# Kernel optimization log

Hardware: AMD Instinct MI355X
Metric: run time of the kernel (lower is better)

Reference implementation:

```python
import jax, jax.numpy as jnp
import numpy as np

N_NODES = 10000
N_EDGES = 640000
NODE_DIM = 128
EDGE_DIM = 32
OUT_DIM = 128


def setup_inputs() -> dict:
    key = jax.random.key(0)
    k_h, k_e, k_ef, k_w1, k_w2 = jax.random.split(key, 5)
    h = jax.random.normal(k_h, (N_NODES, NODE_DIM), dtype=jnp.float32)
    edge_index = jax.random.randint(k_e, (2, N_EDGES), 0, N_NODES, dtype=jnp.int64)
    edge_features = jax.random.normal(k_ef, (N_EDGES, EDGE_DIM), dtype=jnp.float32)
    in_dim = 2 * NODE_DIM + EDGE_DIM
    # Kaiming-ish init scale for realism
    W1 = jax.random.normal(k_w1, (in_dim, OUT_DIM), dtype=jnp.float32) / np.sqrt(in_dim)
    b1 = jnp.zeros((OUT_DIM,), dtype=jnp.float32)
    W2 = jax.random.normal(k_w2, (OUT_DIM, OUT_DIM), dtype=jnp.float32) / np.sqrt(OUT_DIM)
    b2 = jnp.zeros((OUT_DIM,), dtype=jnp.float32)
    return {"h": h, "edge_index": edge_index, "edge_features": edge_features,
            "n": N_NODES, "W1": W1, "b1": b1, "W2": W2, "b2": b2}


def reference(h, edge_index, edge_features, n, W1, b1, W2, b2):
    rows, cols = edge_index[0], edge_index[1]
    # gather source/target node features + edge features -> [E, 2*node_dim+edge_dim]
    msg_input = jnp.concatenate([h[rows], h[cols], edge_features], axis=-1)
    hidden = jax.nn.relu(msg_input @ W1 + b1)   # [E, out_dim]
    messages = hidden @ W2 + b2                 # [E, out_dim]
    # scatter-add messages onto destination rows -> [n, out_dim]
    out = jax.ops.segment_sum(messages, rows, num_segments=n)
    return out
```

## Files before the change

### kernel.cpp

```cpp
#include <hip/hip_runtime.h>
#include <hip/hip_bf16.h>


typedef __attribute__((ext_vector_type(8))) short bf16x8;
typedef __attribute__((ext_vector_type(4))) float f32x4;

#define ND 128
#define ED 32
#define CH 64

__device__ __forceinline__ short f2bf(float x) {
  unsigned int u = __float_as_uint(x);
  unsigned int r = (u + 0x7FFFu + ((u >> 16) & 1u)) >> 16;
  return (short)r;
}

__device__ __forceinline__ float bf2f(short s) {
  return __uint_as_float(((unsigned int)(unsigned short)s) << 16);
}

__device__ __forceinline__ f32x4 bf8lo(bf16x8 v) {
  f32x4 r;
  #pragma unroll
  for (int j = 0; j < 4; ++j) r[j] = bf2f(v[j]);
  return r;
}
__device__ __forceinline__ f32x4 bf8hi(bf16x8 v) {
  f32x4 r;
  #pragma unroll
  for (int j = 0; j < 4; ++j) r[j] = bf2f(v[4 + j]);
  return r;
}

__device__ __forceinline__ int load_idx(const void* ei, long long i, int is64) {
  return is64 ? (int)((const long long*)ei)[i] : ((const int*)ei)[i];
}

__device__ __forceinline__ int swz(int c) {
  int ct = c >> 4, cc = c & 15;
  return (ct >> 2) * 64 + (cc >> 2) * 16 + (ct & 3) * 4 + (cc & 3);
}

__global__ __launch_bounds__(256) void prep_kernel(
    const float* __restrict__ W1, const float* __restrict__ W2,
    const unsigned int* __restrict__ ei, short* __restrict__ w12t,
    short* __restrict__ w1eA, short* __restrict__ w2t, int* __restrict__ flag,
    int* __restrict__ counts, int N) {
  if (blockIdx.x == 0 && threadIdx.x == 0) {
    int is64 = 1;
    for (int i = 0; i < 16; ++i)
      if (ei[2 * i + 1] != 0u) is64 = 0;
    flag[0] = is64;
  }
  int t = blockIdx.x * blockDim.x + threadIdx.x;
  for (int i = t; i < N; i += 32768) counts[i] = 0;
  if (t < 256 * 128) {
    int np = t >> 7, k = t & 127;
    float v = (np < 128) ? W1[k * 128 + np] : W1[(128 + k) * 128 + (np - 128)];
    w12t[t] = f2bf(v);
  }
  if (t < 128 * 128) {
    int n = t >> 7, k = t & 127;
    w2t[t] = f2bf(W2[k * 128 + n]);
  }
  if (t < 8 * 64 * 8) {
    int ct = t >> 9, lane = (t >> 3) & 63, j = t & 7;
    int li = lane & 15, lg = lane >> 4;
    w1eA[t] = f2bf(W1[(256 + lg * 8 + j) * 128 + ct * 16 + li]);
  }
}

__global__ void hist_kernel(const void* __restrict__ ei, const int* __restrict__ flag,
                            int* __restrict__ counts, int* __restrict__ rank,
                            unsigned int* __restrict__ rc, int E) {
  int e = blockIdx.x * blockDim.x + threadIdx.x;
  if (e >= E) return;
  int f = flag[0];
  int r = load_idx(ei, e, f);
  int c = load_idx(ei, (long long)E + e, f);
  rank[e] = atomicAdd(&counts[r], 1);
  rc[e] = ((unsigned int)r << 16) | (unsigned int)c;
}

__global__ __launch_bounds__(1024) void scan_kernel(const int* __restrict__ counts,
                                                    int* __restrict__ row_ptr, int n) {
  __shared__ int wtot[16];
  int tid = threadIdx.x;
  int lane = tid & 63, w = tid >> 6;
  int base_i = tid * 16;
  int c[16];
  int tot = 0;
  #pragma unroll
  for (int j = 0; j < 16; ++j) {
    int i = base_i + j;
    c[j] = (i < n) ? counts[i] : 0;
    tot += c[j];
  }
  int x = tot;
  #pragma unroll
  for (int d = 1; d < 64; d <<= 1) {
    int t = __shfl_up(x, d);
    if (lane >= d) x += t;
  }
  if (lane == 63) wtot[w] = x;
  __syncthreads();
  if (w == 0) {
    int y = (lane < 16) ? wtot[lane] : 0;
    #pragma unroll
    for (int d = 1; d < 16; d <<= 1) {
      int t = __shfl_up(y, d);
      if (lane >= d) y += t;
    }
    if (lane < 16) wtot[lane] = y;
  }
  __syncthreads();
  int waveoff = (w == 0) ? 0 : wtot[w - 1];
  int run = waveoff + x - tot;
  if (tid == 0) row_ptr[0] = 0;
  #pragma unroll
  for (int j = 0; j < 16; ++j) {
    int i = base_i + j;
    if (i < n) {
      run += c[j];
      row_ptr[i + 1] = run;
    }
  }
}

__global__ __launch_bounds__(256, 4) void scatter_sg_kernel(
    const float* __restrict__ ef, const int* __restrict__ row_ptr,
    const int* __restrict__ rank, const unsigned int* __restrict__ rc,
    const float* __restrict__ h, const short* __restrict__ w12t,
    const float* __restrict__ b1, short* __restrict__ efb,
    unsigned short* __restrict__ ccol, int2* __restrict__ cb,
    float* __restrict__ s2, short* __restrict__ g2, int N, int E, int nchunks) {
  int b = blockIdx.x;
  int SGB = (N + 63) >> 6;
  int SCB = (4 * E + 255) >> 8;
  if (b < SGB) {
    int lane = threadIdx.x & 63, w = threadIdx.x >> 6;
    int li = lane & 15, lg = lane >> 4;
    int base = b * 64 + w * 16;
    int rowm = base + li;
    if (rowm >= N) rowm = N - 1;
    float breg[8];
    #pragma unroll
    for (int nt = 0; nt < 8; ++nt) breg[nt] = b1[nt * 16 + li];
    f32x4 acc[16];
    #pragma unroll
    for (int nt = 0; nt < 16; ++nt) acc[nt] = (f32x4){0.f, 0.f, 0.f, 0.f};
    #pragma unroll
    for (int kc = 0; kc < 4; ++kc) {
      f32x4 f0 = *(const f32x4*)(h + (size_t)rowm * ND + kc * 32 + lg * 8);
      f32x4 f1 = *(const f32x4*)(h + (size_t)rowm * ND + kc * 32 + lg * 8 + 4);
      bf16x8 a;
      #pragma unroll
      for (int j = 0; j < 4; ++j) { a[j] = f2bf(f0[j]); a[4 + j] = f2bf(f1[j]); }
      #pragma unroll
      for (int nt = 0; nt < 16; ++nt) {
        bf16x8 bb = *(const bf16x8*)(w12t + (nt * 16 + li) * 128 + kc * 32 + lg * 8);
        acc[nt] = __builtin_amdgcn_mfma_f32_16x16x32_bf16(a, bb, acc[nt], 0, 0, 0);
      }
    }
    #pragma unroll
    for (int nt = 0; nt < 16; ++nt)
      #pragma unroll
      for (int r = 0; r < 4; ++r) {
        int row = base + lg * 4 + r;
        if (row < N) {
          if (nt < 8) {
            s2[(size_t)row * 128 + swz(nt * 16 + li)] = acc[nt][r] + breg[nt];
          } else {
            g2[(size_t)row * 128 + swz((nt - 8) * 16 + li)] = f2bf(acc[nt][r]);
          }
        }
      }
  } else if (b < SGB + SCB) {
    int gt = (b - SGB) * 256 + threadIdx.x;
    int e = gt >> 2, part = gt & 3;
    if (e < E) {
      unsigned int p = rc[e];
      int r = (int)(p >> 16), c = (int)(p & 0xffffu);
      int pos = row_ptr[r] + rank[e];
      f32x4 a0 = *(const f32x4*)(ef + (size_t)e * ED + part * 8);
      f32x4 a1 = *(const f32x4*)(ef + (size_t)e * ED + part * 8 + 4);
      bf16x8 ob;
      #pragma unroll
      for (int j = 0; j < 4; ++j) { ob[j] = f2bf(a0[j]); ob[4 + j] = f2bf(a1[j]); }
      *(bf16x8*)(efb + (size_t)pos * ED + part * 8) = ob;
      if (part == 0) ccol[pos] = (unsigned short)c;
    }
  } else {
    int k = (b - SGB - SCB) * 256 + threadIdx.x;
    if (k < nchunks) {
      int t0 = k * CH, t1 = t0 + CH;
      int lo = 0, hi = N;
      while (lo < hi) { int mid = (lo + hi) >> 1; if (row_ptr[mid] < t0) lo = mid + 1; else hi = mid; }
      int na = lo;
      hi = N;
      while (lo < hi) { int mid = (lo + hi) >> 1; if (row_ptr[mid] < t1) lo = mid + 1; else hi = mid; }
      cb[k] = make_int2(na, lo);
    }
  }
}

__global__ __launch_bounds__(128, 4) void layer1_kernel(
    const float* __restrict__ s2, const short* __restrict__ g2,
    const short* __restrict__ efb, const unsigned short* __restrict__ ccol,
    const short* __restrict__ w1eA, const int* __restrict__ row_ptr,
    const int2* __restrict__ cb, float* __restrict__ hsum) {
  int2 bounds = cb[blockIdx.x];
  int na = bounds.x, nb = bounds.y;
  if (na >= nb) return;
  int lane = threadIdx.x & 63;
  int w = threadIdx.x >> 6;
  int li = lane & 15, lg = lane >> 4;

  bf16x8 wa[4];
  #pragma unroll
  for (int nt = 0; nt < 4; ++nt)
    wa[nt] = *(const bf16x8*)(w1eA + ((w * 4 + nt) * 64 + lane) * 8);

  for (int n = na; n < nb; ++n) {
    int rp = row_ptr[n], rpe = row_ptr[n + 1];
    int deg = rpe - rp;
    f32x4 sreg[4];
    #pragma unroll
    for (int nt = 0; nt < 4; ++nt)
      sreg[nt] = *(const f32x4*)(s2 + (size_t)n * 128 + w * 64 + lg * 16 + nt * 4);
    f32x4 psum[4];
    #pragma unroll
    for (int nt = 0; nt < 4; ++nt) psum[nt] = (f32x4){0.f, 0.f, 0.f, 0.f};

    int ntiles = (deg + 15) >> 4;
    int last = rpe - 1;
    auto ldpos = [&](int t) {
      int p = rp + t * 16 + li;
      return p > last ? last : p;
    };

    int pA = ldpos(0), pB = ldpos(1);
    int cA = ccol[pA], cB = ccol[pB];
    bf16x8 eA = *(const bf16x8*)(efb + (size_t)pA * ED + lg * 8);
    bf16x8 eB = *(const bf16x8*)(efb + (size_t)pB * ED + lg * 8);
    const short* gpA = g2 + (size_t)cA * 128 + w * 64 + lg * 16;
    bf16x8 gA0 = *(const bf16x8*)gpA;
    bf16x8 gA1 = *(const bf16x8*)(gpA + 8);

    for (int t = 0; t < ntiles; ++t) {
      const short* gpB = g2 + (size_t)cB * 128 + w * 64 + lg * 16;
      bf16x8 gB0 = *(const bf16x8*)gpB;
      bf16x8 gB1 = *(const bf16x8*)(gpB + 8);
      int pC = ldpos(t + 2);
      int cC = ccol[pC];
      bf16x8 eC = *(const bf16x8*)(efb + (size_t)pC * ED + lg * 8);
      f32x4 a0 = __builtin_amdgcn_mfma_f32_16x16x32_bf16(wa[0], eA, (f32x4){0.f,0.f,0.f,0.f}, 0, 0, 0);
      f32x4 a1 = __builtin_amdgcn_mfma_f32_16x16x32_bf16(wa[1], eA, (f32x4){0.f,0.f,0.f,0.f}, 0, 0, 0);
      f32x4 a2 = __builtin_amdgcn_mfma_f32_16x16x32_bf16(wa[2], eA, (f32x4){0.f,0.f,0.f,0.f}, 0, 0, 0);
      f32x4 a3 = __builtin_amdgcn_mfma_f32_16x16x32_bf16(wa[3], eA, (f32x4){0.f,0.f,0.f,0.f}, 0, 0, 0);
      if ((t * 16 + li) < deg) {
        f32x4 v0 = a0 + sreg[0] + bf8lo(gA0);
        f32x4 v1 = a1 + sreg[1] + bf8hi(gA0);
        f32x4 v2 = a2 + sreg[2] + bf8lo(gA1);
        f32x4 v3 = a3 + sreg[3] + bf8hi(gA1);
        #pragma unroll
        for (int r = 0; r < 4; ++r) {
          psum[0][r] += (v0[r] > 0.f ? v0[r] : 0.f);
          psum[1][r] += (v1[r] > 0.f ? v1[r] : 0.f);
          psum[2][r] += (v2[r] > 0.f ? v2[r] : 0.f);
          psum[3][r] += (v3[r] > 0.f ? v3[r] : 0.f);
        }
      }
      cB = cC; eA = eB; eB = eC;
      gA0 = gB0; gA1 = gB1;
    }

    #pragma unroll
    for (int nt = 0; nt < 4; ++nt)
      #pragma unroll
      for (int r = 0; r < 4; ++r) {
        float v = psum[nt][r];
        v += __shfl_xor(v, 1);
        v += __shfl_xor(v, 2);
        v += __shfl_xor(v, 4);
        v += __shfl_xor(v, 8);
        psum[nt][r] = v;
      }
    if (li == 0) {
      #pragma unroll
      for (int nt = 0; nt < 4; ++nt)
        *(f32x4*)(hsum + (size_t)n * 128 + w * 64 + nt * 16 + lg * 4) = psum[nt];
    }
  }
}

__global__ __launch_bounds__(256) void out_kernel(const float* __restrict__ hsum,
                                                  const short* __restrict__ w2t,
                                                  const float* __restrict__ b2,
                                                  const int* __restrict__ row_ptr,
                                                  float* __restrict__ out, int N) {
  int lane = threadIdx.x & 63, w = threadIdx.x >> 6;
  int li = lane & 15, lg = lane >> 4;
  int base = blockIdx.x * 64 + w * 16;
  int rowm = base + li;
  if (rowm >= N) rowm = N - 1;
  float breg[8];
  #pragma unroll
  for (int nt = 0; nt < 8; ++nt) breg[nt] = b2[nt * 16 + li];
  f32x4 acc[8];
  #pragma unroll
  for (int nt = 0; nt < 8; ++nt) acc[nt] = (f32x4){0.f, 0.f, 0.f, 0.f};
  #pragma unroll
  for (int kc = 0; kc < 4; ++kc) {
    f32x4 f0 = *(const f32x4*)(hsum + (size_t)rowm * 128 + kc * 32 + lg * 8);
    f32x4 f1 = *(const f32x4*)(hsum + (size_t)rowm * 128 + kc * 32 + lg * 8 + 4);
    bf16x8 a;
    #pragma unroll
    for (int j = 0; j < 4; ++j) { a[j] = f2bf(f0[j]); a[4 + j] = f2bf(f1[j]); }
    #pragma unroll
    for (int nt = 0; nt < 8; ++nt) {
      bf16x8 bb = *(const bf16x8*)(w2t + (nt * 16 + li) * 128 + kc * 32 + lg * 8);
      acc[nt] = __builtin_amdgcn_mfma_f32_16x16x32_bf16(a, bb, acc[nt], 0, 0, 0);
    }
  }
  #pragma unroll
  for (int r = 0; r < 4; ++r) {
    int row = base + lg * 4 + r;
    if (row < N) {
      float dg = (float)(row_ptr[row + 1] - row_ptr[row]);
      #pragma unroll
      for (int nt = 0; nt < 8; ++nt)
        out[(size_t)row * 128 + nt * 16 + li] = acc[nt][r] + dg * breg[nt];
    }
  }
}

extern "C" void kernel_launch(void* const* d_in, const int* in_sizes, int n_in,
                              void* d_out, int out_size, void* d_ws, size_t ws_size,
                              hipStream_t stream) {
  const float* h  = (const float*)d_in[0];
  const void*  ei = d_in[1];
  const float* ef = (const float*)d_in[2];
  const float* W1 = (const float*)d_in[4];
  const float* b1 = (const float*)d_in[5];
  const float* W2 = (const float*)d_in[6];
  const float* b2 = (const float*)d_in[7];
  float* out = (float*)d_out;
  int N = in_sizes[0] / ND;
  int E = in_sizes[2] / ED;
  int nchunks = (E + CH - 1) / CH;

  char* ws = (char*)d_ws;
  size_t off = 0;
  auto alloc = [&](size_t bytes) {
    size_t o = off;
    off = (off + bytes + 255) & ~(size_t)255;
    return o;
  };
  int*            flag    = (int*)(ws + alloc(4));
  int*            counts  = (int*)(ws + alloc((size_t)N * 4));
  int*            row_ptr = (int*)(ws + alloc((size_t)(N + 1) * 4));
  int*            rank    = (int*)(ws + alloc((size_t)E * 4));
  unsigned int*   rc      = (unsigned int*)(ws + alloc((size_t)E * 4));
  short*          w12t    = (short*)(ws + alloc(256 * 128 * 2));
  short*          w1eA    = (short*)(ws + alloc(8 * 64 * 8 * 2));
  short*          w2t     = (short*)(ws + alloc(128 * 128 * 2));
  float*          s2      = (float*)(ws + alloc((size_t)N * 128 * 4));
  short*          g2      = (short*)(ws + alloc((size_t)N * 128 * 2));
  float*          hsumb   = (float*)(ws + alloc((size_t)N * 128 * 4));
  short*          efb     = (short*)(ws + alloc((size_t)E * ED * 2));
  unsigned short* ccol    = (unsigned short*)(ws + alloc((size_t)E * 2));
  int2*           cbb     = (int2*)(ws + alloc((size_t)nchunks * 8));

  int SGB = (N + 63) >> 6;
  int SCB = (4 * E + 255) >> 8;
  int CBB = (nchunks + 255) >> 8;

  prep_kernel<<<128, 256, 0, stream>>>(W1, W2, (const unsigned int*)ei, w12t, w1eA, w2t,
                                       flag, counts, N);
  hist_kernel<<<(E + 255) / 256, 256, 0, stream>>>(ei, flag, counts, rank, rc, E);
  scan_kernel<<<1, 1024, 0, stream>>>(counts, row_ptr, N);
  scatter_sg_kernel<<<SGB + SCB + CBB, 256, 0, stream>>>(
      ef, row_ptr, rank, rc, h, w12t, b1, efb, ccol, cbb, s2, g2, N, E, nchunks);
  layer1_kernel<<<nchunks, 128, 0, stream>>>(s2, g2, efb, ccol, w1eA, row_ptr, cbb, hsumb);
  out_kernel<<<(N + 63) / 64, 256, 0, stream>>>(hsumb, w2t, b2, row_ptr, out, N);
}
```

Measured before the change: 139.1 us.

## Store edge features in FP8, fuse prep with histogram, and use atomic-cursor scatter

Edge features are converted to FP8 instead of bf16 when scattered into CSR order, and the edge-feature part of layer 1 now uses FP8 MFMA with a scaled FP8 copy of the W1 edge slice. This halves the bytes of the edge-feature stream. The weight prep and histogram kernels are merged into one launch, with a memset replacing the in-kernel zeroing. The per-edge rank array is replaced by an atomic cursor per row during the scatter, which drops one E-sized array but makes edge order within a row nondeterministic. FP8 for the edge features and weights lowers accuracy.

```diff
diff --git a/kernel.cpp b/kernel.cpp
--- a/kernel.cpp
+++ b/kernel.cpp
@@ -8,6 +8,7 @@
 #define ND 128
 #define ED 32
 #define CH 64
+#define INV_WSCALE 0.0625f
 
 __device__ __forceinline__ short f2bf(float x) {
   unsigned int u = __float_as_uint(x);
@@ -32,8 +33,10 @@
   return r;
 }
 
-__device__ __forceinline__ int load_idx(const void* ei, long long i, int is64) {
-  return is64 ? (int)((const long long*)ei)[i] : ((const int*)ei)[i];
+__device__ __forceinline__ int pk_fp8x4(float a, float b, float c, float d) {
+  int w = __builtin_amdgcn_cvt_pk_fp8_f32(a, b, 0, false);
+  w = __builtin_amdgcn_cvt_pk_fp8_f32(c, d, w, true);
+  return w;
 }
 
 __device__ __forceinline__ int swz(int c) {
@@ -41,49 +44,60 @@
   return (ct >> 2) * 64 + (cc >> 2) * 16 + (ct & 3) * 4 + (cc & 3);
 }
 
-__global__ __launch_bounds__(256) void prep_kernel(
+__global__ __launch_bounds__(256) void prep_hist_kernel(
     const float* __restrict__ W1, const float* __restrict__ W2,
-    const unsigned int* __restrict__ ei, short* __restrict__ w12t,
-    short* __restrict__ w1eA, short* __restrict__ w2t, int* __restrict__ flag,
-    int* __restrict__ counts, int N) {
-  if (blockIdx.x == 0 && threadIdx.x == 0) {
-    int is64 = 1;
-    for (int i = 0; i < 16; ++i)
-      if (ei[2 * i + 1] != 0u) is64 = 0;
-    flag[0] = is64;
-  }
-  int t = blockIdx.x * blockDim.x + threadIdx.x;
-  for (int i = t; i < N; i += 32768) counts[i] = 0;
-  if (t < 256 * 128) {
-    int np = t >> 7, k = t & 127;
-    float v = (np < 128) ? W1[k * 128 + np] : W1[(128 + k) * 128 + (np - 128)];
-    w12t[t] = f2bf(v);
-  }
-  if (t < 128 * 128) {
-    int n = t >> 7, k = t & 127;
-    w2t[t] = f2bf(W2[k * 128 + n]);
-  }
-  if (t < 8 * 64 * 8) {
-    int ct = t >> 9, lane = (t >> 3) & 63, j = t & 7;
-    int li = lane & 15, lg = lane >> 4;
-    w1eA[t] = f2bf(W1[(256 + lg * 8 + j) * 128 + ct * 16 + li]);
-  }
-}
-
-__global__ void hist_kernel(const void* __restrict__ ei, const int* __restrict__ flag,
-                            int* __restrict__ counts, int* __restrict__ rank,
-                            unsigned int* __restrict__ rc, int E) {
-  int e = blockIdx.x * blockDim.x + threadIdx.x;
-  if (e >= E) return;
-  int f = flag[0];
-  int r = load_idx(ei, e, f);
-  int c = load_idx(ei, (long long)E + e, f);
-  rank[e] = atomicAdd(&counts[r], 1);
-  rc[e] = ((unsigned int)r << 16) | (unsigned int)c;
+    const void* __restrict__ ei, int* __restrict__ counts,
+    unsigned int* __restrict__ rc, short* __restrict__ w12t,
+    long long* __restrict__ w1eA8, short* __restrict__ w2t, int E) {
+  int b = blockIdx.x;
+  if (b < 128) {
+    int t = b * 256 + threadIdx.x;
+    if (t < 256 * 128) {
+      int np = t >> 7, k = t & 127;
+      float v = (np < 128) ? W1[k * 128 + np] : W1[(128 + k) * 128 + (np - 128)];
+      w12t[t] = f2bf(v);
+    }
+    if (t < 128 * 128) {
+      int n = t >> 7, k = t & 127;
+      w2t[t] = f2bf(W2[k * 128 + n]);
+    }
+    if (t < 8 * 64) {
+      int ct = t >> 6, lane = t & 63;
+      int li = lane & 15, lg = lane >> 4;
+      float v[8];
+      #pragma unroll
+      for (int j = 0; j < 8; ++j)
+        v[j] = W1[(256 + lg * 8 + j) * 128 + ct * 16 + li] * 16.f;
+      int lo = pk_fp8x4(v[0], v[1], v[2], v[3]);
+      int hi = pk_fp8x4(v[4], v[5], v[6], v[7]);
+      w1eA8[ct * 64 + lane] = (long long)(unsigned int)lo |
+                              ((long long)(unsigned int)hi << 32);
+    }
+  } else {
+    int e = (b - 128) * 256 + threadIdx.x;
+    if (e < E) {
+      const unsigned int* u = (const unsigned int*)ei;
+      int is64 = 1;
+      #pragma unroll
+      for (int i = 0; i < 16; ++i)
+        if (u[2 * i + 1] != 0u) is64 = 0;
+      int r, c;
+      if (is64) {
+        r = (int)((const long long*)ei)[e];
+        c = (int)((const long long*)ei)[(long long)E + e];
+      } else {
+        r = ((const int*)ei)[e];
+        c = ((const int*)ei)[E + e];
+      }
+      atomicAdd(&counts[r], 1);
+      rc[e] = ((unsigned int)r << 16) | (unsigned int)c;
+    }
+  }
 }
 
 __global__ __launch_bounds__(1024) void scan_kernel(const int* __restrict__ counts,
-                                                    int* __restrict__ row_ptr, int n) {
+                                                    int* __restrict__ row_ptr,
+                                                    int* __restrict__ cur, int n) {
   __shared__ int wtot[16];
   int tid = threadIdx.x;
   int lane = tid & 63, w = tid >> 6;
@@ -121,6 +135,7 @@
   for (int j = 0; j < 16; ++j) {
     int i = base_i + j;
     if (i < n) {
+      cur[i] = run;
       run += c[j];
       row_ptr[i + 1] = run;
     }
@@ -129,14 +144,14 @@
 
 __global__ __launch_bounds__(256, 4) void scatter_sg_kernel(
     const float* __restrict__ ef, const int* __restrict__ row_ptr,
-    const int* __restrict__ rank, const unsigned int* __restrict__ rc,
+    int* __restrict__ cur, const unsigned int* __restrict__ rc,
     const float* __restrict__ h, const short* __restrict__ w12t,
-    const float* __restrict__ b1, short* __restrict__ efb,
+    const float* __restrict__ b1, unsigned char* __restrict__ efb,
     unsigned short* __restrict__ ccol, int2* __restrict__ cb,
     float* __restrict__ s2, short* __restrict__ g2, int N, int E, int nchunks) {
   int b = blockIdx.x;
   int SGB = (N + 63) >> 6;
-  int SCB = (4 * E + 255) >> 8;
+  int SCB = (2 * E + 255) >> 8;
   if (b < SGB) {
     int lane = threadIdx.x & 63, w = threadIdx.x >> 6;
     int li = lane & 15, lg = lane >> 4;
@@ -177,17 +192,25 @@
       }
   } else if (b < SGB + SCB) {
     int gt = (b - SGB) * 256 + threadIdx.x;
-    int e = gt >> 2, part = gt & 3;
+    int e = gt >> 1, part = gt & 1;
     if (e < E) {
       unsigned int p = rc[e];
       int r = (int)(p >> 16), c = (int)(p & 0xffffu);
-      int pos = row_ptr[r] + rank[e];
-      f32x4 a0 = *(const f32x4*)(ef + (size_t)e * ED + part * 8);
-      f32x4 a1 = *(const f32x4*)(ef + (size_t)e * ED + part * 8 + 4);
-      bf16x8 ob;
-      #pragma unroll
-      for (int j = 0; j < 4; ++j) { ob[j] = f2bf(a0[j]); ob[4 + j] = f2bf(a1[j]); }
-      *(bf16x8*)(efb + (size_t)pos * ED + part * 8) = ob;
+      int pos0 = 0;
+      if (part == 0) pos0 = atomicAdd(&cur[r], 1);
+      int lane = threadIdx.x & 63;
+      int pos = __shfl(pos0, lane - part);
+      const float* ep = ef + (size_t)e * ED + part * 16;
+      f32x4 x0 = *(const f32x4*)(ep);
+      f32x4 x1 = *(const f32x4*)(ep + 4);
+      f32x4 x2 = *(const f32x4*)(ep + 8);
+      f32x4 x3 = *(const f32x4*)(ep + 12);
+      int4 ob;
+      ob.x = pk_fp8x4(x0[0], x0[1], x0[2], x0[3]);
+      ob.y = pk_fp8x4(x1[0], x1[1], x1[2], x1[3]);
+      ob.z = pk_fp8x4(x2[0], x2[1], x2[2], x2[3]);
+      ob.w = pk_fp8x4(x3[0], x3[1], x3[2], x3[3]);
+      *(int4*)(efb + (size_t)pos * ED + part * 16) = ob;
       if (part == 0) ccol[pos] = (unsigned short)c;
     }
   } else {
@@ -206,8 +229,8 @@
 
 __global__ __launch_bounds__(128, 4) void layer1_kernel(
     const float* __restrict__ s2, const short* __restrict__ g2,
-    const short* __restrict__ efb, const unsigned short* __restrict__ ccol,
-    const short* __restrict__ w1eA, const int* __restrict__ row_ptr,
+    const unsigned char* __restrict__ efb, const unsigned short* __restrict__ ccol,
+    const long long* __restrict__ w1eA8, const int* __restrict__ row_ptr,
     const int2* __restrict__ cb, float* __restrict__ hsum) {
   int2 bounds = cb[blockIdx.x];
   int na = bounds.x, nb = bounds.y;
@@ -216,10 +239,10 @@
   int w = threadIdx.x >> 6;
   int li = lane & 15, lg = lane >> 4;
 
-  bf16x8 wa[4];
+  long long wa[4];
   #pragma unroll
   for (int nt = 0; nt < 4; ++nt)
-    wa[nt] = *(const bf16x8*)(w1eA + ((w * 4 + nt) * 64 + lane) * 8);
+    wa[nt] = w1eA8[(w * 4 + nt) * 64 + lane];
 
   for (int n = na; n < nb; ++n) {
     int rp = row_ptr[n], rpe = row_ptr[n + 1];
@@ -241,8 +264,8 @@
 
     int pA = ldpos(0), pB = ldpos(1);
     int cA = ccol[pA], cB = ccol[pB];
-    bf16x8 eA = *(const bf16x8*)(efb + (size_t)pA * ED + lg * 8);
-    bf16x8 eB = *(const bf16x8*)(efb + (size_t)pB * ED + lg * 8);
+    long long eA = *(const long long*)(efb + (size_t)pA * ED + lg * 8);
+    long long eB = *(const long long*)(efb + (size_t)pB * ED + lg * 8);
     const short* gpA = g2 + (size_t)cA * 128 + w * 64 + lg * 16;
     bf16x8 gA0 = *(const bf16x8*)gpA;
     bf16x8 gA1 = *(const bf16x8*)(gpA + 8);
@@ -253,22 +276,23 @@
       bf16x8 gB1 = *(const bf16x8*)(gpB + 8);
       int pC = ldpos(t + 2);
       int cC = ccol[pC];
-      bf16x8 eC = *(const bf16x8*)(efb + (size_t)pC * ED + lg * 8);
-      f32x4 a0 = __builtin_amdgcn_mfma_f32_16x16x32_bf16(wa[0], eA, (f32x4){0.f,0.f,0.f,0.f}, 0, 0, 0);
-      f32x4 a1 = __builtin_amdgcn_mfma_f32_16x16x32_bf16(wa[1], eA, (f32x4){0.f,0.f,0.f,0.f}, 0, 0, 0);
-      f32x4 a2 = __builtin_amdgcn_mfma_f32_16x16x32_bf16(wa[2], eA, (f32x4){0.f,0.f,0.f,0.f}, 0, 0, 0);
-      f32x4 a3 = __builtin_amdgcn_mfma_f32_16x16x32_bf16(wa[3], eA, (f32x4){0.f,0.f,0.f,0.f}, 0, 0, 0);
+      long long eC = *(const long long*)(efb + (size_t)pC * ED + lg * 8);
+      f32x4 a0 = __builtin_amdgcn_mfma_f32_16x16x32_fp8_fp8(wa[0], eA, (f32x4){0.f,0.f,0.f,0.f}, 0, 0, 0);
+      f32x4 a1 = __builtin_amdgcn_mfma_f32_16x16x32_fp8_fp8(wa[1], eA, (f32x4){0.f,0.f,0.f,0.f}, 0, 0, 0);
+      f32x4 a2 = __builtin_amdgcn_mfma_f32_16x16x32_fp8_fp8(wa[2], eA, (f32x4){0.f,0.f,0.f,0.f}, 0, 0, 0);
+      f32x4 a3 = __builtin_amdgcn_mfma_f32_16x16x32_fp8_fp8(wa[3], eA, (f32x4){0.f,0.f,0.f,0.f}, 0, 0, 0);
       if ((t * 16 + li) < deg) {
-        f32x4 v0 = a0 + sreg[0] + bf8lo(gA0);
-        f32x4 v1 = a1 + sreg[1] + bf8hi(gA0);
-        f32x4 v2 = a2 + sreg[2] + bf8lo(gA1);
-        f32x4 v3 = a3 + sreg[3] + bf8hi(gA1);
+        f32x4 g0 = bf8lo(gA0), g1 = bf8hi(gA0), g2v = bf8lo(gA1), g3 = bf8hi(gA1);
         #pragma unroll
         for (int r = 0; r < 4; ++r) {
-          psum[0][r] += (v0[r] > 0.f ? v0[r] : 0.f);
-          psum[1][r] += (v1[r] > 0.f ? v1[r] : 0.f);
-          psum[2][r] += (v2[r] > 0.f ? v2[r] : 0.f);
-          psum[3][r] += (v3[r] > 0.f ? v3[r] : 0.f);
+          float v0 = fmaf(a0[r], INV_WSCALE, sreg[0][r] + g0[r]);
+          float v1 = fmaf(a1[r], INV_WSCALE, sreg[1][r] + g1[r]);
+          float v2 = fmaf(a2[r], INV_WSCALE, sreg[2][r] + g2v[r]);
+          float v3 = fmaf(a3[r], INV_WSCALE, sreg[3][r] + g3[r]);
+          psum[0][r] += (v0 > 0.f ? v0 : 0.f);
+          psum[1][r] += (v1 > 0.f ? v1 : 0.f);
+          psum[2][r] += (v2 > 0.f ? v2 : 0.f);
+          psum[3][r] += (v3 > 0.f ? v3 : 0.f);
         }
       }
       cB = cC; eA = eB; eB = eC;
@@ -357,31 +381,30 @@
     off = (off + bytes + 255) & ~(size_t)255;
     return o;
   };
-  int*            flag    = (int*)(ws + alloc(4));
   int*            counts  = (int*)(ws + alloc((size_t)N * 4));
   int*            row_ptr = (int*)(ws + alloc((size_t)(N + 1) * 4));
-  int*            rank    = (int*)(ws + alloc((size_t)E * 4));
+  int*            cur     = (int*)(ws + alloc((size_t)N * 4));
   unsigned int*   rc      = (unsigned int*)(ws + alloc((size_t)E * 4));
   short*          w12t    = (short*)(ws + alloc(256 * 128 * 2));
-  short*          w1eA    = (short*)(ws + alloc(8 * 64 * 8 * 2));
+  long long*      w1eA8   = (long long*)(ws + alloc(8 * 64 * 8));
   short*          w2t     = (short*)(ws + alloc(128 * 128 * 2));
   float*          s2      = (float*)(ws + alloc((size_t)N * 128 * 4));
   short*          g2      = (short*)(ws + alloc((size_t)N * 128 * 2));
   float*          hsumb   = (float*)(ws + alloc((size_t)N * 128 * 4));
-  short*          efb     = (short*)(ws + alloc((size_t)E * ED * 2));
+  unsigned char*  efb     = (unsigned char*)(ws + alloc((size_t)E * ED));
   unsigned short* ccol    = (unsigned short*)(ws + alloc((size_t)E * 2));
   int2*           cbb     = (int2*)(ws + alloc((size_t)nchunks * 8));
 
   int SGB = (N + 63) >> 6;
-  int SCB = (4 * E + 255) >> 8;
+  int SCB = (2 * E + 255) >> 8;
   int CBB = (nchunks + 255) >> 8;
 
-  prep_kernel<<<128, 256, 0, stream>>>(W1, W2, (const unsigned int*)ei, w12t, w1eA, w2t,
-                                       flag, counts, N);
-  hist_kernel<<<(E + 255) / 256, 256, 0, stream>>>(ei, flag, counts, rank, rc, E);
-  scan_kernel<<<1, 1024, 0, stream>>>(counts, row_ptr, N);
+  hipMemsetAsync(counts, 0, (size_t)N * 4, stream);
+  prep_hist_kernel<<<128 + (E + 255) / 256, 256, 0, stream>>>(
+      W1, W2, ei, counts, rc, w12t, w1eA8, w2t, E);
+  scan_kernel<<<1, 1024, 0, stream>>>(counts, row_ptr, cur, N);
   scatter_sg_kernel<<<SGB + SCB + CBB, 256, 0, stream>>>(
-      ef, row_ptr, rank, rc, h, w12t, b1, efb, ccol, cbb, s2, g2, N, E, nchunks);
-  layer1_kernel<<<nchunks, 128, 0, stream>>>(s2, g2, efb, ccol, w1eA, row_ptr, cbb, hsumb);
+      ef, row_ptr, cur, rc, h, w12t, b1, efb, ccol, cbb, s2, g2, N, E, nchunks);
+  layer1_kernel<<<nchunks, 128, 0, stream>>>(s2, g2, efb, ccol, w1eA8, row_ptr, cbb, hsumb);
   out_kernel<<<(N + 63) / 64, 256, 0, stream>>>(hsumb, w2t, b2, row_ptr, out, N);
 }
```

Measured after the change: 158.7 us. 14.1% more time.
